# Kernel optimization log

Measured on AMD Instinct MI355X. Metric: run time of the kernel, lower is better.

Reference implementation:

```python
import jax, jax.numpy as jnp
import numpy as np

NUDGE = 1e-7

def _norm(x):
    # global mean + L2-norm over axes (1,2), per sample (faithful to source)
    size = x.shape[1] * x.shape[2]
    mean = jnp.sum(x, axis=(1, 2), keepdims=True) / size
    xc = x - mean
    l2 = jnp.sqrt(jnp.sum(xc * xc, axis=(1, 2), keepdims=True))
    return xc / (l2 + NUDGE)


def setup_inputs() -> dict:
    key = jax.random.key(0)
    ks = jax.random.split(key, 9)
    B, D, S, F = 8, 512, 4096, 2048
    s = 0.02
    x = jax.random.normal(ks[0], (B, D, S), dtype=jnp.float32)
    Wq = jax.random.normal(ks[1], (D, D), dtype=jnp.float32) * s
    Wk = jax.random.normal(ks[2], (D, D), dtype=jnp.float32) * s
    Wv = jax.random.normal(ks[3], (D, D), dtype=jnp.float32) * s
    Wo = jax.random.normal(ks[4], (D, D), dtype=jnp.float32) * s
    W1 = jax.random.normal(ks[5], (D, F), dtype=jnp.float32) * s
    b1 = jnp.zeros((F,), dtype=jnp.float32)
    W2 = jax.random.normal(ks[6], (F, D), dtype=jnp.float32) * s
    b2 = jnp.zeros((D,), dtype=jnp.float32)
    return {"x": x, "Wq": Wq, "Wk": Wk, "Wv": Wv, "Wo": Wo,
            "W1": W1, "b1": b1, "W2": W2, "b2": b2}


def reference(x, Wq, Wk, Wv, Wo, W1, b1, W2, b2):
    B, D, S = x.shape
    xt = jnp.swapaxes(x, 1, 2)                      # [B,S,D]
    q = xt @ Wq                                     # [B,S,D]
    k = xt @ Wk
    v = xt @ Wv
    scores = jnp.einsum('bsd,btd->bst', q, k) / jnp.sqrt(jnp.float32(D))
    attn = jax.nn.softmax(scores, axis=-1)          # [B,S,S]
    attn_out = jnp.swapaxes((attn @ v) @ Wo, 1, 2)  # [B,D,S]

    post = _norm(x + attn_out)                      # [B,D,S]

    # per-slice feedforward+linear loop == batched matmul over token axis
    pt = jnp.swapaxes(post, 1, 2)                   # [B,S,D]
    h = jax.nn.relu(pt @ W1 + b1) @ W2 + b2         # [B,S,D]
    return _norm(post + jnp.swapaxes(h, 1, 2))
```

## Files before the change

kernel.cpp:

```cpp
#include <hip/hip_runtime.h>


typedef unsigned short u16;
typedef __attribute__((ext_vector_type(4))) float f32x4;
typedef __attribute__((ext_vector_type(8))) short s16x8;

__device__ __forceinline__ float bf2f(u16 u) {
    unsigned int v = ((unsigned int)u) << 16;
    float f;
    __builtin_memcpy(&f, &v, 4);
    return f;
}
__device__ __forceinline__ u16 f2bf(float f) {
    unsigned int v;
    __builtin_memcpy(&v, &f, 4);
    unsigned int r = (v + 0x7fffu + ((v >> 16) & 1u)) >> 16;
    return (u16)r;
}
__device__ __forceinline__ u16 loadbf(const void* p, long long i, int f32) {
    return f32 ? f2bf(((const float*)p)[i]) : ((const u16*)p)[i];
}

#if defined(__has_builtin)
#if __has_builtin(__builtin_amdgcn_global_load_lds)
#define HAS_GLDS 1
#endif
#endif
#ifndef HAS_GLDS
#define HAS_GLDS 0
#endif

#if HAS_GLDS
__device__ __forceinline__ void glds16(const u16* g, u16* l) {
    __builtin_amdgcn_global_load_lds(
        (const __attribute__((address_space(1))) void*)g,
        (__attribute__((address_space(3))) void*)l, 16, 0, 0);
}
#endif

__global__ __launch_bounds__(256) void detect_f32(
    const u16* __restrict__ p, int n_u16, int* __restrict__ flag)
{
    int insane = 0;
    for (int i = threadIdx.x; i < n_u16; i += 256) {
        u16 h = p[i];
        int e = (h >> 7) & 0xFF;
        int m = h & 0x7F;
        bool sane = (e >= 96 && e <= 141) || (e == 0 && m == 0);
        insane += sane ? 0 : 1;
    }
#pragma unroll
    for (int off = 32; off > 0; off >>= 1) insane += __shfl_down(insane, off);
    __shared__ int red[4];
    if ((threadIdx.x & 63) == 0) red[threadIdx.x >> 6] = insane;
    __syncthreads();
    if (threadIdx.x == 0)
        *flag = (red[0] + red[1] + red[2] + red[3] > n_u16 / 4) ? 1 : 0;
}

#define BM 128
#define BN 128
#define BK 32

template <typename OutT, bool BIAS, bool RELU>
__global__ __launch_bounds__(256) void gemm_bt(
    const u16* __restrict__ A, const u16* __restrict__ Bt, OutT* __restrict__ C,
    const u16* __restrict__ bias, int M, int N, int K,
    int lda, int ldb, int ldc, int wmod,
    long long aZ, long long aW, long long bZ, long long bW, long long cZ)
{
    __shared__ u16 As[BM * BK];
    __shared__ u16 Bs[BN * BK];

    const int z = blockIdx.z;
    const int g = z / wmod, w = z - g * wmod;
    A  += g * aZ + w * aW;
    Bt += g * bZ + w * bW;
    C  += (long long)z * cZ;

    const int tid = threadIdx.x;
    const int bx = blockIdx.x, by = blockIdx.y;
    const int wave = tid >> 6, lane = tid & 63;
    const int wm = wave >> 1, wn = wave & 1;
    const int q = lane >> 4, r = lane & 15;

    const int ar = tid >> 2;
    const int ac = (tid & 3) * 8;

    const u16* Ag = A + (long long)(by * BM + ar) * lda + ac;
    const u16* Bg = Bt + (long long)(bx * BN + ar) * ldb + ac;
    const long long rstepA = 64LL * lda, rstepB = 64LL * ldb;

    f32x4 acc[4][4];
    const f32x4 zero = {0.f, 0.f, 0.f, 0.f};
#pragma unroll
    for (int i = 0; i < 4; ++i)
#pragma unroll
        for (int j = 0; j < 4; ++j) acc[i][j] = zero;

    for (int k0 = 0; k0 < K; k0 += BK) {
#if HAS_GLDS
        glds16(Ag, &As[tid * 8]);
        glds16(Ag + rstepA, &As[2048 + tid * 8]);
        glds16(Bg, &Bs[tid * 8]);
        glds16(Bg + rstepB, &Bs[2048 + tid * 8]);
        Ag += BK; Bg += BK;
        __syncthreads();
#else
        int4 a0 = *(const int4*)(Ag);
        int4 a1 = *(const int4*)(Ag + rstepA);
        int4 b0 = *(const int4*)(Bg);
        int4 b1 = *(const int4*)(Bg + rstepB);
        Ag += BK; Bg += BK;
        __syncthreads();
        *(int4*)(&As[tid * 8]) = a0;
        *(int4*)(&As[2048 + tid * 8]) = a1;
        *(int4*)(&Bs[tid * 8]) = b0;
        *(int4*)(&Bs[2048 + tid * 8]) = b1;
        __syncthreads();
#endif
        s16x8 af[4], bf[4];
#pragma unroll
        for (int mi = 0; mi < 4; ++mi)
            af[mi] = *(const s16x8*)(&As[(wm * 64 + mi * 16 + r) * BK + q * 8]);
#pragma unroll
        for (int ni = 0; ni < 4; ++ni)
            bf[ni] = *(const s16x8*)(&Bs[(wn * 64 + ni * 16 + r) * BK + q * 8]);
#pragma unroll
        for (int mi = 0; mi < 4; ++mi)
#pragma unroll
            for (int ni = 0; ni < 4; ++ni)
                acc[mi][ni] = __builtin_amdgcn_mfma_f32_16x16x32_bf16(
                    af[mi], bf[ni], acc[mi][ni], 0, 0, 0);
#if HAS_GLDS
        __syncthreads();
#endif
    }

    const int col0 = bx * BN + wn * 64;
    const int row0 = by * BM + wm * 64;
#pragma unroll
    for (int ni = 0; ni < 4; ++ni) {
        const int colg = col0 + ni * 16 + r;
        float bv = 0.f;
        if constexpr (BIAS) bv = bf2f(bias[colg]);
#pragma unroll
        for (int mi = 0; mi < 4; ++mi) {
#pragma unroll
            for (int rr = 0; rr < 4; ++rr) {
                const int rowg = row0 + mi * 16 + q * 4 + rr;
                float v = acc[mi][ni][rr] + bv;
                if constexpr (RELU) v = fmaxf(v, 0.f);
                if constexpr (sizeof(OutT) == 2)
                    C[(long long)rowg * ldc + colg] = (OutT)f2bf(v);
                else
                    C[(long long)rowg * ldc + colg] = (OutT)v;
            }
        }
    }
}

__global__ __launch_bounds__(256) void transpose_any(
    const void* __restrict__ in, u16* __restrict__ out, int R, int C,
    long long sIn, long long sOut, const int* __restrict__ flag)
{
    __shared__ u16 tile[32][33];
    const int f32 = *flag;
    const long long ib = (long long)blockIdx.z * sIn;
    u16* ob = out + (long long)blockIdx.z * sOut;
    const int c0 = blockIdx.x * 32, r0 = blockIdx.y * 32;
    const int tx = threadIdx.x, ty = threadIdx.y;
#pragma unroll
    for (int i = 0; i < 4; ++i) {
        int rr = ty + i * 8;
        tile[rr][tx] = loadbf(in, ib + (long long)(r0 + rr) * C + c0 + tx, f32);
    }
    __syncthreads();
#pragma unroll
    for (int i = 0; i < 4; ++i) {
        int cc = ty + i * 8;
        ob[(long long)(c0 + cc) * R + r0 + tx] = tile[tx][cc];
    }
}

__global__ __launch_bounds__(256) void transpose_b16(
    const u16* __restrict__ in, u16* __restrict__ out, int R, int C,
    long long sIn, long long sOut)
{
    __shared__ u16 tile[32][33];
    in += (long long)blockIdx.z * sIn;
    out += (long long)blockIdx.z * sOut;
    const int c0 = blockIdx.x * 32, r0 = blockIdx.y * 32;
    const int tx = threadIdx.x, ty = threadIdx.y;
#pragma unroll
    for (int i = 0; i < 4; ++i) {
        int rr = ty + i * 8;
        tile[rr][tx] = in[(long long)(r0 + rr) * C + c0 + tx];
    }
    __syncthreads();
#pragma unroll
    for (int i = 0; i < 4; ++i) {
        int cc = ty + i * 8;
        out[(long long)(c0 + cc) * R + r0 + tx] = tile[tx][cc];
    }
}

__global__ __launch_bounds__(256) void convert_bias(
    const void* __restrict__ b1, const void* __restrict__ b2,
    u16* __restrict__ ob, const int* __restrict__ f1, const int* __restrict__ f2)
{
    int i = blockIdx.x * 256 + threadIdx.x;
    if (i < 2048) ob[i] = loadbf(b1, i, *f1);
    else if (i < 2560) ob[i] = loadbf(b2, i - 2048, *f2);
}

__global__ __launch_bounds__(256) void softmax_bf16(u16* __restrict__ sc)
{
    const float scale = 0.044194173824159216f;
    u16* row = sc + (long long)blockIdx.x * 4096;
    const int tid = threadIdx.x, lane = tid & 63, wave = tid >> 6;

    u16 h[16];
    *(int4*)(h) = ((const int4*)row)[tid];
    *(int4*)(h + 8) = ((const int4*)row)[tid + 256];
    float v[16];
    float m = -3.4e38f;
#pragma unroll
    for (int j = 0; j < 16; ++j) {
        v[j] = bf2f(h[j]) * scale;
        m = fmaxf(m, v[j]);
    }
#pragma unroll
    for (int off = 32; off > 0; off >>= 1) m = fmaxf(m, __shfl_down(m, off));
    __shared__ float redm[4], reds[4];
    if (lane == 0) redm[wave] = m;
    __syncthreads();
    m = fmaxf(fmaxf(redm[0], redm[1]), fmaxf(redm[2], redm[3]));

    float s = 0.f;
#pragma unroll
    for (int j = 0; j < 16; ++j) { v[j] = __expf(v[j] - m); s += v[j]; }
#pragma unroll
    for (int off = 32; off > 0; off >>= 1) s += __shfl_down(s, off);
    if (lane == 0) reds[wave] = s;
    __syncthreads();
    s = reds[0] + reds[1] + reds[2] + reds[3];
    const float inv = 1.f / s;
#pragma unroll
    for (int j = 0; j < 16; ++j) h[j] = f2bf(v[j] * inv);
    ((int4*)row)[tid] = *(const int4*)(h);
    ((int4*)row)[tid + 256] = *(const int4*)(h + 8);
}

__global__ __launch_bounds__(256) void reduce_legs(
    const float* __restrict__ P, u16* __restrict__ O, int legs)
{
    const long long SD = 4096LL * 512;
    const int g = blockIdx.y;
    const float* Pg = P + (long long)g * legs * SD;
    u16* Og = O + (long long)g * SD;
    const int base = blockIdx.x * 2048;
#pragma unroll
    for (int it = 0; it < 8; ++it) {
        int i = base + it * 256 + threadIdx.x;
        float s = 0.f;
        for (int l = 0; l < legs; ++l) s += Pg[(long long)l * SD + i];
        Og[i] = f2bf(s);
    }
}

__global__ __launch_bounds__(256) void stats_add_partial(
    const u16* __restrict__ A, const u16* __restrict__ Bv,
    float2* __restrict__ partial)
{
    const int b = blockIdx.y;
    const long long yb = (long long)b * (4096LL * 512);
    const int base = blockIdx.x * 2048;
    float s = 0.f, ss = 0.f;
#pragma unroll
    for (int it = 0; it < 8; ++it) {
        int i = base + it * 256 + threadIdx.x;
        float z = bf2f(A[yb + i]) + bf2f(Bv[yb + i]);
        s += z; ss += z * z;
    }
#pragma unroll
    for (int off = 32; off > 0; off >>= 1) {
        s += __shfl_down(s, off); ss += __shfl_down(ss, off);
    }
    __shared__ float red[8];
    int lane = threadIdx.x & 63, wave = threadIdx.x >> 6;
    if (lane == 0) { red[wave * 2] = s; red[wave * 2 + 1] = ss; }
    __syncthreads();
    if (threadIdx.x == 0) {
        for (int w = 1; w < 4; ++w) { s += red[w * 2]; ss += red[w * 2 + 1]; }
        partial[b * 1024 + blockIdx.x] = make_float2(s, ss);
    }
}

__global__ __launch_bounds__(256) void stats_finish(
    const float2* __restrict__ partial, float2* __restrict__ stats, float N)
{
    const int b = blockIdx.x;
    float s = 0.f, ss = 0.f;
    for (int i = threadIdx.x; i < 1024; i += 256) {
        float2 p = partial[b * 1024 + i];
        s += p.x; ss += p.y;
    }
#pragma unroll
    for (int off = 32; off > 0; off >>= 1) {
        s += __shfl_down(s, off); ss += __shfl_down(ss, off);
    }
    __shared__ float red[8];
    int lane = threadIdx.x & 63, wave = threadIdx.x >> 6;
    if (lane == 0) { red[wave * 2] = s; red[wave * 2 + 1] = ss; }
    __syncthreads();
    if (threadIdx.x == 0) {
        for (int w = 1; w < 4; ++w) { s += red[w * 2]; ss += red[w * 2 + 1]; }
        float mean = s / N;
        float l2 = sqrtf(fmaxf(ss - s * s / N, 0.f));
        stats[b] = make_float2(mean, 1.f / (l2 + 1e-7f));
    }
}

__global__ __launch_bounds__(256) void post_kernel(
    const u16* __restrict__ A, const u16* __restrict__ Bv,
    const float2* __restrict__ stats, u16* __restrict__ post)
{
    const int b = blockIdx.y;
    const float2 st = stats[b];
    const long long yb = (long long)b * (4096LL * 512);
    const int base = blockIdx.x * 2048;
#pragma unroll
    for (int it = 0; it < 8; ++it) {
        int i = base + it * 256 + threadIdx.x;
        float z = bf2f(A[yb + i]) + bf2f(Bv[yb + i]);
        post[yb + i] = f2bf((z - st.x) * st.y);
    }
}

__global__ __launch_bounds__(256) void final_kernel(
    const u16* __restrict__ P, const u16* __restrict__ G,
    const float2* __restrict__ stats, float* __restrict__ out)
{
    __shared__ float tile[32][33];
    const int b = blockIdx.z;
    const float2 st = stats[b];
    const long long bb = (long long)b * (4096LL * 512);
    const int s0 = blockIdx.x * 32, d0 = blockIdx.y * 32;
    const int tx = threadIdx.x, ty = threadIdx.y;
#pragma unroll
    for (int i = 0; i < 4; ++i) {
        int sl = ty + i * 8;
        long long idx = bb + (long long)(s0 + sl) * 512 + d0 + tx;
        tile[sl][tx] = bf2f(P[idx]) + bf2f(G[idx]);
    }
    __syncthreads();
#pragma unroll
    for (int i = 0; i < 4; ++i) {
        int dl = ty + i * 8;
        out[bb + (long long)(d0 + dl) * 4096 + s0 + tx] =
            (tile[tx][dl] - st.x) * st.y;
    }
}

extern "C" void kernel_launch(void* const* d_in, const int* in_sizes, int n_in,
                              void* d_out, int out_size, void* d_ws, size_t ws_size,
                              hipStream_t stream)
{
    (void)out_size;
    const void* x  = d_in[0];
    const void* Wq = d_in[1];
    const void* Wk = d_in[2];
    const void* Wv = d_in[3];
    const void* Wo = d_in[4];
    const void* W1 = d_in[5];
    const void* b1 = d_in[6];
    const void* W2 = d_in[7];
    const void* b2 = d_in[8];

    const int Bb = 8, D = 512, S = 4096, F = 2048;
    const long long SD = (long long)S * D;
    const long long DD = (long long)D * D;
    const long long SS = (long long)S * S;

    char* ws = (char*)d_ws;
    size_t off = 0;
    auto take = [&](size_t bytes) -> char* {
        char* p = ws + off;
        off += (bytes + 255) & ~(size_t)255;
        return p;
    };
    u16* xt   = (u16*)take((size_t)Bb * SD * 2);
    u16* WqT  = (u16*)take((size_t)DD * 2);
    u16* WkT  = (u16*)take((size_t)DD * 2);
    u16* WvT  = (u16*)take((size_t)DD * 2);
    u16* WoT  = (u16*)take((size_t)DD * 2);
    u16* W1T  = (u16*)take((size_t)D * F * 2);
    u16* W2T  = (u16*)take((size_t)D * F * 2);
    u16* bb   = (u16*)take(2560 * 2);
    u16* post = (u16*)take((size_t)Bb * SD * 2);
    float2* npart  = (float2*)take(8 * 1024 * sizeof(float2));
    float2* stats1v = (float2*)take(256);
    float2* stats2v = (float2*)take(256);
    int* flags = (int*)take(16 * sizeof(int));

    size_t remaining = ws_size > off ? ws_size - off : 0;
    const size_t perG = (size_t)4 * SD * 2 + (size_t)SS * 2 + 65536;
    int G = (remaining >= 8 * perG) ? 8 : (remaining >= 4 * perG) ? 4
          : (remaining >= 2 * perG) ? 2 : 1;
    int legs = (G == 1) ? 4 : (G == 2) ? 2 : 1;

    u16* QKV    = (u16*)take((size_t)3 * G * SD * 2);
    u16* Vt     = (u16*)take((size_t)G * SD * 2);
    u16* scores = (u16*)take((size_t)G * SS * 2);
    float* partK = (float*)post;
    u16* Oall = (u16*)d_out;
    u16* Y    = scores;
    u16* Hbuf = (u16*)d_out;
    u16* Gbuf = scores;

    for (int i = 0; i < 9 && i < n_in; ++i) {
        int n = in_sizes[i] < 8192 ? in_sizes[i] : 8192;
        detect_f32<<<1, 256, 0, stream>>>((const u16*)d_in[i], n, flags + i);
    }

    dim3 tb(32, 8, 1);
    transpose_any<<<dim3(S / 32, D / 32, Bb), tb, 0, stream>>>(x, xt, D, S, SD, SD, flags + 0);
    transpose_any<<<dim3(16, 16, 1), tb, 0, stream>>>(Wq, WqT, D, D, 0, 0, flags + 1);
    transpose_any<<<dim3(16, 16, 1), tb, 0, stream>>>(Wk, WkT, D, D, 0, 0, flags + 2);
    transpose_any<<<dim3(16, 16, 1), tb, 0, stream>>>(Wv, WvT, D, D, 0, 0, flags + 3);
    transpose_any<<<dim3(16, 16, 1), tb, 0, stream>>>(Wo, WoT, D, D, 0, 0, flags + 4);
    transpose_any<<<dim3(F / 32, D / 32, 1), tb, 0, stream>>>(W1, W1T, D, F, 0, 0, flags + 5);
    transpose_any<<<dim3(D / 32, F / 32, 1), tb, 0, stream>>>(W2, W2T, F, D, 0, 0, flags + 7);
    convert_bias<<<10, 256, 0, stream>>>(b1, b2, bb, flags + 6, flags + 8);

    for (int b0 = 0; b0 < Bb; b0 += G) {
        gemm_bt<u16, false, false><<<dim3(D / 128, S / 128, 3 * G), 256, 0, stream>>>(
            xt + (long long)b0 * SD, WqT, QKV, nullptr, S, D, D, D, D, D,
            3, SD, 0, 0, DD, SD);
        transpose_b16<<<dim3(D / 32, S / 32, G), tb, 0, stream>>>(
            QKV + 2 * SD, Vt, S, D, 3 * SD, SD);
        gemm_bt<u16, false, false><<<dim3(S / 128, S / 128, G), 256, 0, stream>>>(
            QKV, QKV + SD, scores, nullptr, S, S, D, D, D, S,
            1, 3 * SD, 0, 3 * SD, 0, SS);
        softmax_bf16<<<dim3(G * S), 256, 0, stream>>>(scores);
        if (legs == 1) {
            gemm_bt<u16, false, false><<<dim3(D / 128, S / 128, G), 256, 0, stream>>>(
                scores, Vt, Oall + (long long)b0 * SD, nullptr, S, D, S, S, S, D,
                1, SS, 0, SD, 0, SD);
        } else {
            gemm_bt<float, false, false><<<dim3(D / 128, S / 128, G * legs), 256, 0, stream>>>(
                scores, Vt, partK, nullptr, S, D, S / legs, S, S, D,
                legs, SS, S / legs, SD, S / legs, SD);
            reduce_legs<<<dim3(1024, G), 256, 0, stream>>>(
                partK, Oall + (long long)b0 * SD, legs);
        }
    }

    gemm_bt<u16, false, false><<<dim3(D / 128, (Bb * S) / 128, 1), 256, 0, stream>>>(
        Oall, WoT, Y, nullptr, Bb * S, D, D, D, D, D, 1, 0, 0, 0, 0, 0);

    stats_add_partial<<<dim3(1024, Bb), 256, 0, stream>>>(xt, Y, npart);
    stats_finish<<<dim3(Bb), 256, 0, stream>>>(npart, stats1v, (float)SD);
    post_kernel<<<dim3(1024, Bb), 256, 0, stream>>>(xt, Y, stats1v, post);

    for (int h = 0; h < 2; ++h) {
        gemm_bt<u16, true, true><<<dim3(F / 128, (4 * S) / 128, 1), 256, 0, stream>>>(
            post + (long long)h * 4 * SD, W1T, Hbuf, bb, 4 * S, F, D, D, D, F,
            1, 0, 0, 0, 0, 0);
        gemm_bt<u16, true, false><<<dim3(D / 128, (4 * S) / 128, 1), 256, 0, stream>>>(
            Hbuf, W2T, Gbuf + (long long)h * 4 * SD, bb + 2048, 4 * S, D, F, F, F, D,
            1, 0, 0, 0, 0, 0);
    }

    stats_add_partial<<<dim3(1024, Bb), 256, 0, stream>>>(post, Gbuf, npart);
    stats_finish<<<dim3(Bb), 256, 0, stream>>>(npart, stats2v, (float)SD);
    final_kernel<<<dim3(S / 32, D / 32, Bb), tb, 0, stream>>>(
        post, Gbuf, stats2v, (float*)d_out);
}
```

Before: 1.230 ms.

## Double-buffer GEMM LDS tiles and swizzle score-GEMM blocks across XCDs

The bf16 GEMM now keeps two LDS buffers and issues the global-to-LDS loads for the next K tile before running the MFMAs on the current one. This overlaps memory latency with compute and drops one barrier per iteration. The QK^T scores GEMM also remaps its block indices so that consecutive blocks dispatched to the same XCD share rows, which should improve L2 reuse. Costs are doubled LDS use (32KB per block), which may lower occupancy, and a swizzle hardcoded to a 32x32 grid.

```diff
diff --git a/kernel.cpp b/kernel.cpp
--- a/kernel.cpp
+++ b/kernel.cpp
@@ -67,10 +67,11 @@
     const u16* __restrict__ A, const u16* __restrict__ Bt, OutT* __restrict__ C,
     const u16* __restrict__ bias, int M, int N, int K,
     int lda, int ldb, int ldc, int wmod,
-    long long aZ, long long aW, long long bZ, long long bW, long long cZ)
-{
-    __shared__ u16 As[BM * BK];
-    __shared__ u16 Bs[BN * BK];
+    long long aZ, long long aW, long long bZ, long long bW, long long cZ,
+    int swz)
+{
+    __shared__ u16 As[2][BM * BK];
+    __shared__ u16 Bs[2][BN * BK];
 
     const int z = blockIdx.z;
     const int g = z / wmod, w = z - g * wmod;
@@ -78,8 +79,15 @@
     Bt += g * bZ + w * bW;
     C  += (long long)z * cZ;
 
+    int bx = blockIdx.x, by = blockIdx.y;
+    if (swz) {
+        int id = by * 32 + bx;
+        int xcd = id & 7, i = id >> 3;
+        by = xcd * 4 + (i & 3);
+        bx = i >> 2;
+    }
+
     const int tid = threadIdx.x;
-    const int bx = blockIdx.x, by = blockIdx.y;
     const int wave = tid >> 6, lane = tid & 63;
     const int wm = wave >> 1, wn = wave & 1;
     const int q = lane >> 4, r = lane & 15;
@@ -98,44 +106,72 @@
 #pragma unroll
         for (int j = 0; j < 4; ++j) acc[i][j] = zero;
 
-    for (int k0 = 0; k0 < K; k0 += BK) {
+    const int nIter = K / BK;
 #if HAS_GLDS
-        glds16(Ag, &As[tid * 8]);
-        glds16(Ag + rstepA, &As[2048 + tid * 8]);
-        glds16(Bg, &Bs[tid * 8]);
-        glds16(Bg + rstepB, &Bs[2048 + tid * 8]);
-        Ag += BK; Bg += BK;
-        __syncthreads();
-#else
-        int4 a0 = *(const int4*)(Ag);
-        int4 a1 = *(const int4*)(Ag + rstepA);
-        int4 b0 = *(const int4*)(Bg);
-        int4 b1 = *(const int4*)(Bg + rstepB);
-        Ag += BK; Bg += BK;
-        __syncthreads();
-        *(int4*)(&As[tid * 8]) = a0;
-        *(int4*)(&As[2048 + tid * 8]) = a1;
-        *(int4*)(&Bs[tid * 8]) = b0;
-        *(int4*)(&Bs[2048 + tid * 8]) = b1;
-        __syncthreads();
-#endif
+    glds16(Ag, &As[0][tid * 8]);
+    glds16(Ag + rstepA, &As[0][2048 + tid * 8]);
+    glds16(Bg, &Bs[0][tid * 8]);
+    glds16(Bg + rstepB, &Bs[0][2048 + tid * 8]);
+    Ag += BK; Bg += BK;
+    __syncthreads();
+    for (int it = 0; it < nIter; ++it) {
+        const int cur = it & 1, nxt = cur ^ 1;
+        if (it + 1 < nIter) {
+            glds16(Ag, &As[nxt][tid * 8]);
+            glds16(Ag + rstepA, &As[nxt][2048 + tid * 8]);
+            glds16(Bg, &Bs[nxt][tid * 8]);
+            glds16(Bg + rstepB, &Bs[nxt][2048 + tid * 8]);
+            Ag += BK; Bg += BK;
+        }
         s16x8 af[4], bf[4];
 #pragma unroll
         for (int mi = 0; mi < 4; ++mi)
-            af[mi] = *(const s16x8*)(&As[(wm * 64 + mi * 16 + r) * BK + q * 8]);
+            af[mi] = *(const s16x8*)(&As[cur][(wm * 64 + mi * 16 + r) * BK + q * 8]);
 #pragma unroll
         for (int ni = 0; ni < 4; ++ni)
-            bf[ni] = *(const s16x8*)(&Bs[(wn * 64 + ni * 16 + r) * BK + q * 8]);
+            bf[ni] = *(const s16x8*)(&Bs[cur][(wn * 64 + ni * 16 + r) * BK + q * 8]);
 #pragma unroll
         for (int mi = 0; mi < 4; ++mi)
 #pragma unroll
             for (int ni = 0; ni < 4; ++ni)
                 acc[mi][ni] = __builtin_amdgcn_mfma_f32_16x16x32_bf16(
                     af[mi], bf[ni], acc[mi][ni], 0, 0, 0);
-#if HAS_GLDS
         __syncthreads();
+    }
+#else
+    int4 a0 = *(const int4*)(Ag);
+    int4 a1 = *(const int4*)(Ag + rstepA);
+    int4 b0 = *(const int4*)(Bg);
+    int4 b1 = *(const int4*)(Bg + rstepB);
+    for (int it = 0; it < nIter; ++it) {
+        __syncthreads();
+        *(int4*)(&As[0][tid * 8]) = a0;
+        *(int4*)(&As[0][2048 + tid * 8]) = a1;
+        *(int4*)(&Bs[0][tid * 8]) = b0;
+        *(int4*)(&Bs[0][2048 + tid * 8]) = b1;
+        __syncthreads();
+        if (it + 1 < nIter) {
+            Ag += BK; Bg += BK;
+            a0 = *(const int4*)(Ag);
+            a1 = *(const int4*)(Ag + rstepA);
+            b0 = *(const int4*)(Bg);
+            b1 = *(const int4*)(Bg + rstepB);
+        }
+        s16x8 af[4], bf[4];
+#pragma unroll
+        for (int mi = 0; mi < 4; ++mi)
+            af[mi] = *(const s16x8*)(&As[0][(wm * 64 + mi * 16 + r) * BK + q * 8]);
+#pragma unroll
+        for (int ni = 0; ni < 4; ++ni)
+            bf[ni] = *(const s16x8*)(&Bs[0][(wn * 64 + ni * 16 + r) * BK + q * 8]);
+#pragma unroll
+        for (int mi = 0; mi < 4; ++mi)
+#pragma unroll
+            for (int ni = 0; ni < 4; ++ni)
+                acc[mi][ni] = __builtin_amdgcn_mfma_f32_16x16x32_bf16(
+                    af[mi], bf[ni], acc[mi][ni], 0, 0, 0);
+    }
 #endif
-    }
 
     const int col0 = bx * BN + wn * 64;
     const int row0 = by * BM + wm * 64;
@@ -437,28 +473,28 @@
     for (int b0 = 0; b0 < Bb; b0 += G) {
         gemm_bt<u16, false, false><<<dim3(D / 128, S / 128, 3 * G), 256, 0, stream>>>(
             xt + (long long)b0 * SD, WqT, QKV, nullptr, S, D, D, D, D, D,
-            3, SD, 0, 0, DD, SD);
+            3, SD, 0, 0, DD, SD, 0);
         transpose_b16<<<dim3(D / 32, S / 32, G), tb, 0, stream>>>(
             QKV + 2 * SD, Vt, S, D, 3 * SD, SD);
         gemm_bt<u16, false, false><<<dim3(S / 128, S / 128, G), 256, 0, stream>>>(
             QKV, QKV + SD, scores, nullptr, S, S, D, D, D, S,
-            1, 3 * SD, 0, 3 * SD, 0, SS);
+            1, 3 * SD, 0, 3 * SD, 0, SS, 1 );
         softmax_bf16<<<dim3(G * S), 256, 0, stream>>>(scores);
         if (legs == 1) {
             gemm_bt<u16, false, false><<<dim3(D / 128, S / 128, G), 256, 0, stream>>>(
                 scores, Vt, Oall + (long long)b0 * SD, nullptr, S, D, S, S, S, D,
-                1, SS, 0, SD, 0, SD);
+                1, SS, 0, SD, 0, SD, 0);
         } else {
             gemm_bt<float, false, false><<<dim3(D / 128, S / 128, G * legs), 256, 0, stream>>>(
                 scores, Vt, partK, nullptr, S, D, S / legs, S, S, D,
-                legs, SS, S / legs, SD, S / legs, SD);
+                legs, SS, S / legs, SD, S / legs, SD, 0);
             reduce_legs<<<dim3(1024, G), 256, 0, stream>>>(
                 partK, Oall + (long long)b0 * SD, legs);
         }
     }
 
     gemm_bt<u16, false, false><<<dim3(D / 128, (Bb * S) / 128, 1), 256, 0, stream>>>(
-        Oall, WoT, Y, nullptr, Bb * S, D, D, D, D, D, 1, 0, 0, 0, 0, 0);
+        Oall, WoT, Y, nullptr, Bb * S, D, D, D, D, D, 1, 0, 0, 0, 0, 0, 0);
 
     stats_add_partial<<<dim3(1024, Bb), 256, 0, stream>>>(xt, Y, npart);
     stats_finish<<<dim3(Bb), 256, 0, stream>>>(npart, stats1v, (float)SD);
@@ -467,10 +503,10 @@
     for (int h = 0; h < 2; ++h) {
         gemm_bt<u16, true, true><<<dim3(F / 128, (4 * S) / 128, 1), 256, 0, stream>>>(
             post + (long long)h * 4 * SD, W1T, Hbuf, bb, 4 * S, F, D, D, D, F,
-            1, 0, 0, 0, 0, 0);
+            1, 0, 0, 0, 0, 0, 0);
         gemm_bt<u16, true, false><<<dim3(D / 128, (4 * S) / 128, 1), 256, 0, stream>>>(
             Hbuf, W2T, Gbuf + (long long)h * 4 * SD, bb + 2048, 4 * S, D, F, F, F, D,
-            1, 0, 0, 0, 0, 0);
+            1, 0, 0, 0, 0, 0, 0);
     }
 
     stats_add_partial<<<dim3(1024, Bb), 256, 0, stream>>>(post, Gbuf, npart);
```

Measured after the change: 1.160 ms. 1.06x faster.
